# Kernel tuning notes

Measured on AMD Instinct MI355X. Metric: run time of the kernel, lower is better.

Reference implementation:

```python
import jax, jax.numpy as jnp
import numpy as np
import math

B, T, C, H = 4, 2048, 1024, 16
DH = C // H  # 64

def setup_inputs() -> dict:
    key = jax.random.key(0)
    k1, k2, k3 = jax.random.split(key, 3)
    x = jax.random.normal(k1, (B, T, C), dtype=jnp.float32)
    # standard RoPE angle table: [T, DH/2]
    inv_freq = 1.0 / (10000.0 ** (jnp.arange(0, DH, 2, dtype=jnp.float32) / DH))
    ang = jnp.arange(T, dtype=jnp.float32)[:, None] * inv_freq[None, :]
    cos = jnp.cos(ang)
    sin = jnp.sin(ang)
    Wqkv = jax.random.normal(k2, (3 * C, C), dtype=jnp.float32) * (C ** -0.5)
    Wo = jax.random.normal(k3, (C, C), dtype=jnp.float32) * (C ** -0.5)
    return {"x": x, "cos": cos, "sin": sin, "Wqkv": Wqkv, "Wo": Wo}

def apply_rotary(x, cos, sin):
    # x: [B,H,T,DH]; cos/sin: [T, DH/2] broadcast over B,H
    x1, x2 = x[..., ::2], x[..., 1::2]
    xr = jnp.stack([x1 * cos - x2 * sin, x1 * sin + x2 * cos], axis=-1)
    return xr.reshape(x.shape)

def reference(x, cos, sin, Wqkv, Wo):
    Bz, Tz, Cz = x.shape
    qkv = x @ Wqkv.T  # [B,T,3C]
    q, k, v = jnp.split(qkv, 3, axis=-1)
    def heads(t):
        return t.reshape(Bz, Tz, H, DH).transpose(0, 2, 1, 3)  # [B,H,T,DH]
    q, k, v = heads(q), heads(k), heads(v)
    q = apply_rotary(q, cos, sin)
    k = apply_rotary(k, cos, sin)
    attn = jnp.einsum('bhqd,bhkd->bhqk', q, k) / math.sqrt(DH)
    causal = jnp.tril(jnp.ones((Tz, Tz), dtype=bool))
    attn = jnp.where(causal, attn, jnp.float32(-jnp.inf))
    attn = jax.nn.softmax(attn, axis=-1)
    y = jnp.einsum('bhqk,bhkd->bhqd', attn, v)
    y = y.transpose(0, 2, 1, 3).reshape(Bz, Tz, Cz)
    return y @ Wo.T
```

## Files before the change

kernel.cpp:

```cpp
#include <hip/hip_runtime.h>
#include <math.h>

#define Bz 4
#define Tz 2048
#define Cz 1024
#define Hz 16
#define DHz 64
#define Mz (Bz*Tz)

typedef __attribute__((ext_vector_type(8))) short short8;
typedef __attribute__((ext_vector_type(4))) float f32x4;
typedef __attribute__((ext_vector_type(4))) float flt4;
typedef unsigned long long u64;

__device__ inline unsigned short f2bf(float f){
  union { float f; unsigned int u; } x; x.f = f;
  unsigned int r = x.u + 0x7fffu + ((x.u >> 16) & 1u);
  return (unsigned short)(r >> 16);
}
__device__ inline float bf2f(unsigned short b){
  union { unsigned int u; float f; } x; x.u = ((unsigned int)b) << 16; return x.f;
}
__device__ inline unsigned int packbf2(float lo, float hi){
  union { float f; unsigned int u; } a, b; a.f = lo; b.f = hi;
  return __builtin_amdgcn_perm(b.u, a.u, 0x07060302u);
}

__device__ inline void gload_lds16(const unsigned short* g, char* l){
  __builtin_amdgcn_global_load_lds((const __attribute__((address_space(1))) unsigned int*)g,
                                   (__attribute__((address_space(3))) unsigned int*)l,
                                   16, 0, 0);
}

#define NXE 8388608
#define NW1 3145728
#define NW2 1048576
__global__ __launch_bounds__(256) void cvt_all(const float* __restrict__ x,
                                               const float* __restrict__ wq,
                                               const float* __restrict__ wo,
                                               unsigned short* __restrict__ xb,
                                               unsigned short* __restrict__ wqb,
                                               unsigned short* __restrict__ wob){
  int i = (blockIdx.x * 256 + threadIdx.x) * 4;
  const float* s; unsigned short* d;
  if (i < NXE){ s = x + i; d = xb + i; }
  else if (i < NXE + NW1){ s = wq + (i - NXE); d = wqb + (i - NXE); }
  else { s = wo + (i - NXE - NW1); d = wob + (i - NXE - NW1); }
  flt4 v = *(const flt4*)s;
  u64 pack = (u64)f2bf(v.x) | ((u64)f2bf(v.y) << 16)
           | ((u64)f2bf(v.z) << 32) | ((u64)f2bf(v.w) << 48);
  *(u64*)d = pack;
}

template<int EPI>
__global__ __launch_bounds__(256)
void gemm_bt(const unsigned short* __restrict__ A, const unsigned short* __restrict__ Bw,
             const int K,
             unsigned short* __restrict__ qd, unsigned short* __restrict__ kd,
             unsigned short* __restrict__ vd, float* __restrict__ outf)
{
  __shared__ __align__(16) char lds[32768];
  char* At = lds;
  char* Bt = lds + 16384;

  const int tid  = threadIdx.x;
  const int lane = tid & 63, wid = tid >> 6;
  const int l16  = lane & 15, lg = lane >> 4;
  const int wr   = wid >> 1, wc = wid & 1;
  const int m0   = blockIdx.y * 128, n0 = blockIdx.x * 128;

  f32x4 acc[4][4] = {};
  const int nk = K >> 6;

  for (int kt = 0; kt < nk; ++kt){
    const unsigned short* As = A  + (size_t)m0 * K + kt * 64;
    const unsigned short* Bs = Bw + (size_t)n0 * K + kt * 64;
    #pragma unroll
    for (int it = 0; it < 4; ++it){
      int id  = it * 256 + tid;
      int row = id >> 3, c = id & 7;
      int sc  = c ^ (row & 7);
      char* dA = At + (it * 256 + wid * 64) * 16;
      char* dB = Bt + (it * 256 + wid * 64) * 16;
      gload_lds16(As + (size_t)row * K + sc * 8, dA);
      gload_lds16(Bs + (size_t)row * K + sc * 8, dB);
    }
    __syncthreads();

    #pragma unroll
    for (int ks = 0; ks < 2; ++ks){
      short8 af[4], bf[4];
      #pragma unroll
      for (int mt = 0; mt < 4; ++mt){
        int row = wr * 64 + mt * 16 + l16;
        af[mt] = *(const short8*)(At + row * 128 + (((ks * 4 + lg) ^ (row & 7)) << 4));
      }
      #pragma unroll
      for (int nt = 0; nt < 4; ++nt){
        int row = wc * 64 + nt * 16 + l16;
        bf[nt] = *(const short8*)(Bt + row * 128 + (((ks * 4 + lg) ^ (row & 7)) << 4));
      }
      #pragma unroll
      for (int mt = 0; mt < 4; ++mt)
        #pragma unroll
        for (int nt = 0; nt < 4; ++nt)
          acc[mt][nt] = __builtin_amdgcn_mfma_f32_16x16x32_bf16(af[mt], bf[nt], acc[mt][nt], 0, 0, 0);
    }
    __syncthreads();
  }

  if (EPI == 1){
    #pragma unroll
    for (int mt = 0; mt < 4; ++mt)
      #pragma unroll
      for (int nt = 0; nt < 4; ++nt)
        #pragma unroll
        for (int i = 0; i < 4; ++i){
          int m = m0 + wr * 64 + mt * 16 + lg * 4 + i;
          int n = n0 + wc * 64 + nt * 16 + l16;
          outf[(size_t)m * 1024 + n] = acc[mt][nt][i];
        }
  } else {
    const int part = n0 >> 10;
    if (part < 2){
      unsigned short* dst = part ? kd : qd;
      #pragma unroll
      for (int mt = 0; mt < 4; ++mt)
        #pragma unroll
        for (int nt = 0; nt < 4; ++nt)
          #pragma unroll
          for (int i = 0; i < 4; ++i){
            int m = m0 + wr * 64 + mt * 16 + lg * 4 + i;
            int n = (n0 & 1023) + wc * 64 + nt * 16 + l16;
            int h = n >> 6, d = n & 63;
            int b = m >> 11, t = m & 2047;
            dst[(((size_t)(b * Hz + h)) * Tz + t) * DHz + d] = f2bf(acc[mt][nt][i]);
          }
    } else {
      #pragma unroll
      for (int mt = 0; mt < 4; ++mt)
        #pragma unroll
        for (int nt = 0; nt < 4; ++nt){
          int m = m0 + wr * 64 + mt * 16 + lg * 4;
          int n = (n0 & 1023) + wc * 64 + nt * 16 + l16;
          int h = n >> 6, d = n & 63;
          int b = m >> 11, t = m & 2047;
          u64 w = (u64)f2bf(acc[mt][nt][0]) | ((u64)f2bf(acc[mt][nt][1]) << 16)
                | ((u64)f2bf(acc[mt][nt][2]) << 32) | ((u64)f2bf(acc[mt][nt][3]) << 48);
          *(u64*)(vd + (((size_t)(b * Hz + h)) * DHz + d) * Tz + t) = w;
        }
    }
  }
}

__global__ __launch_bounds__(256) void rope_kernel(unsigned short* __restrict__ qh,
                                                   unsigned short* __restrict__ kh,
                                                   const float* __restrict__ cosb,
                                                   const float* __restrict__ sinb){
  unsigned int idx = blockIdx.x * 256 + threadIdx.x;
  int quad = idx & 7;
  int row  = (idx >> 3) & 131071;
  int buf  = idx >> 20;
  unsigned short* p = (buf ? kh : qh) + (size_t)row * DHz + quad * 8;
  int t = row & (Tz - 1);
  flt4 c = *(const flt4*)(cosb + t * 32 + quad * 4);
  flt4 s = *(const flt4*)(sinb + t * 32 + quad * 4);
  short8 v = *(const short8*)p;
  const float qs = 0.125f * 1.4426950408889634f;
  float sc = buf ? 1.0f : qs;
  short8 o;
  #pragma unroll
  for (int j = 0; j < 4; ++j){
    float x1 = bf2f((unsigned short)v[2*j]);
    float x2 = bf2f((unsigned short)v[2*j+1]);
    float r1 = (x1 * c[j] - x2 * s[j]) * sc;
    float r2 = (x1 * s[j] + x2 * c[j]) * sc;
    o[2*j]   = (short)f2bf(r1);
    o[2*j+1] = (short)f2bf(r2);
  }
  *(short8*)p = o;
}

__global__ __launch_bounds__(256)
void attn_fwd(const unsigned short* __restrict__ qh, const unsigned short* __restrict__ kh,
              const unsigned short* __restrict__ vt, unsigned short* __restrict__ y)
{
  __shared__ __align__(16) char lds[2*8192 + 2*8192 + 4*2304];
  const int tid  = threadIdx.x;
  const int lane = tid & 63, wid = tid >> 6;
  const int l16  = lane & 15, lg = lane >> 4;
  const int bh   = blockIdx.x;
  const int qt   = 31 - blockIdx.y;

  const size_t base = (size_t)bh * Tz * DHz;
  const unsigned short* qb = qh + base;
  const unsigned short* kb = kh + base;
  const unsigned short* vb = vt + base;

  const int qrow = qt * 64 + wid * 16 + l16;
  short8 qf[2];
  qf[0] = *(const short8*)(qb + (size_t)qrow * DHz + 0  + lg * 8);
  qf[1] = *(const short8*)(qb + (size_t)qrow * DHz + 32 + lg * 8);

  const int x07 = l16 & 7;
  const int fo0 = l16 * 128 + (((0 + lg) ^ x07) << 4);
  const int fo1 = l16 * 128 + (((4 + lg) ^ x07) << 4);
  char* const Pb  = (char*)lds + 32768 + wid * 2304;
  const int pwo = (l16 * 72 + lg * 4) * 2;
  const int pro = (l16 * 72 + lg * 8) * 2;

  const int srow = tid >> 3;
  const int scol = (tid & 7) ^ (srow & 7);
  const int kOff = srow * DHz + scol * 8;
  const size_t vOff = (size_t)srow * Tz + scol * 8;

  auto STAGE = [&](int kt, int c){
    const unsigned short* Ks = kb + (size_t)kt * 64 * DHz;
    const unsigned short* Vs = vb + kt * 64;
    char* KD = (char*)lds + c * 8192;
    char* VD = (char*)lds + 16384 + c * 8192;
    #pragma unroll
    for (int it = 0; it < 2; ++it){
      gload_lds16(Ks + kOff + it * 32 * DHz, KD + it * 4096 + wid * 1024);
      gload_lds16(Vs + vOff + (size_t)it * 32 * Tz, VD + it * 4096 + wid * 1024);
    }
  };

  short8 ones;
  #pragma unroll
  for (int j = 0; j < 8; ++j) ones[j] = (short)0x3F80;

  f32x4 o[4] = {};
  f32x4 lsum = {};
  float m_r = -INFINITY;

  int cur = 0;
  STAGE(0, 0);
  __syncthreads();

  for (int kt = 0; kt <= qt; ++kt){
    if (kt < qt) STAGE(kt + 1, cur ^ 1);

    const char* KL = (const char*)lds + cur * 8192;
    const char* VL = (const char*)lds + 16384 + cur * 8192;

    f32x4 s[4] = {};
    __builtin_amdgcn_s_setprio(1);
    #pragma unroll
    for (int nt = 0; nt < 4; ++nt){
      short8 kf = *(const short8*)(KL + fo0 + nt * 2048);
      s[nt] = __builtin_amdgcn_mfma_f32_16x16x32_bf16(kf, qf[0], s[nt], 0, 0, 0);
    }
    #pragma unroll
    for (int nt = 0; nt < 4; ++nt){
      short8 kf = *(const short8*)(KL + fo1 + nt * 2048);
      s[nt] = __builtin_amdgcn_mfma_f32_16x16x32_bf16(kf, qf[1], s[nt], 0, 0, 0);
    }
    __builtin_amdgcn_s_setprio(0);

    if (kt == qt){
      #pragma unroll
      for (int nt = 0; nt < 4; ++nt)
        #pragma unroll
        for (int r = 0; r < 4; ++r){
          int kv = kt * 64 + nt * 16 + lg * 4 + r;
          if (kv > qrow) s[nt][r] = -INFINITY;
        }
    }

    float mx = fmaxf(fmaxf(fmaxf(fmaxf(s[0][0], s[0][1]), fmaxf(s[0][2], s[0][3])),
                           fmaxf(fmaxf(s[1][0], s[1][1]), fmaxf(s[1][2], s[1][3]))),
                     fmaxf(fmaxf(fmaxf(s[2][0], s[2][1]), fmaxf(s[2][2], s[2][3])),
                           fmaxf(fmaxf(s[3][0], s[3][1]), fmaxf(s[3][2], s[3][3]))));
    mx = fmaxf(mx, __shfl_xor(mx, 16));
    mx = fmaxf(mx, __shfl_xor(mx, 32));

    if (!__all(mx - m_r <= 8.0f)){
      float mn = fmaxf(m_r, mx);
      float al = __builtin_amdgcn_exp2f(m_r - mn);
      #pragma unroll
      for (int nt = 0; nt < 4; ++nt)
        #pragma unroll
        for (int i = 0; i < 4; ++i) o[nt][i] *= al;
      #pragma unroll
      for (int i = 0; i < 4; ++i) lsum[i] *= al;
      m_r = mn;
    }

    #pragma unroll
    for (int nt = 0; nt < 4; ++nt){
      float p0 = __builtin_amdgcn_exp2f(s[nt][0] - m_r);
      float p1 = __builtin_amdgcn_exp2f(s[nt][1] - m_r);
      float p2 = __builtin_amdgcn_exp2f(s[nt][2] - m_r);
      float p3 = __builtin_amdgcn_exp2f(s[nt][3] - m_r);
      u64 w = (u64)packbf2(p0, p1) | ((u64)packbf2(p2, p3) << 32);
      *(u64*)(Pb + pwo + nt * 32) = w;
    }

    __builtin_amdgcn_s_setprio(1);
    #pragma unroll
    for (int ks = 0; ks < 2; ++ks){
      short8 pa = *(const short8*)(Pb + pro + ks * 64);
      lsum = __builtin_amdgcn_mfma_f32_16x16x32_bf16(ones, pa, lsum, 0, 0, 0);
      const int fo = ks ? fo1 : fo0;
      #pragma unroll
      for (int nt = 0; nt < 4; ++nt){
        short8 vf = *(const short8*)(VL + fo + nt * 2048);
        o[nt] = __builtin_amdgcn_mfma_f32_16x16x32_bf16(vf, pa, o[nt], 0, 0, 0);
      }
    }
    __builtin_amdgcn_s_setprio(0);

    __syncthreads();
    cur ^= 1;
  }

  const int b = bh >> 4, h = bh & 15;
  const int row = qt * 64 + wid * 16 + l16;
  unsigned short* yb = y + ((size_t)b * Tz + row) * Cz + h * 64 + lg * 4;
  float inv = 1.f / lsum[0];
  #pragma unroll
  for (int nt = 0; nt < 4; ++nt){
    u64 w = (u64)f2bf(o[nt][0] * inv) | ((u64)f2bf(o[nt][1] * inv) << 16)
          | ((u64)f2bf(o[nt][2] * inv) << 32) | ((u64)f2bf(o[nt][3] * inv) << 48);
    *(u64*)(yb + nt * 16) = w;
  }
}

extern "C" void kernel_launch(void* const* d_in, const int* in_sizes, int n_in,
                              void* d_out, int out_size, void* d_ws, size_t ws_size,
                              hipStream_t stream)
{
  const float* x    = (const float*)d_in[0];
  const float* cosb = (const float*)d_in[1];
  const float* sinb = (const float*)d_in[2];
  const float* Wqkv = (const float*)d_in[3];
  const float* Wo   = (const float*)d_in[4];
  float* out = (float*)d_out;

  char* ws = (char*)d_ws;
  unsigned short* xb    = (unsigned short*)(ws);
  unsigned short* ybuf  = xb;
  unsigned short* wqkvb = (unsigned short*)(ws + 16777216);
  unsigned short* wob   = (unsigned short*)(ws + 23068672);
  unsigned short* qhb   = (unsigned short*)(ws + 25165824);
  unsigned short* khb   = (unsigned short*)(ws + 41943040);
  unsigned short* vtb   = (unsigned short*)(ws + 58720256);

  cvt_all<<<12288, 256, 0, stream>>>(x, Wqkv, Wo, xb, wqkvb, wob);

  dim3 g1(24, 64);
  gemm_bt<0><<<g1, 256, 0, stream>>>(xb, wqkvb, Cz, qhb, khb, vtb, nullptr);

  rope_kernel<<<8192, 256, 0, stream>>>(qhb, khb, cosb, sinb);

  dim3 g2(64, 32);
  attn_fwd<<<g2, 256, 0, stream>>>(qhb, khb, vtb, ybuf);

  dim3 g3(8, 64);
  gemm_bt<1><<<g3, 256, 0, stream>>>(ybuf, wob, Cz, nullptr, nullptr, nullptr, out);
}
```

Baseline: 266.2 us.

## Fuse RoPE into QKV GEMM epilogue, swizzle block order, vectorize stores

Drops the standalone RoPE kernel and applies rotary embedding plus the Q scale in the QKV GEMM epilogue. Swapped MFMA operands give each lane contiguous columns, which allows packed 8-byte bf16 and 16-byte fp32 stores. All three main kernels use a 1D grid with an XCD-aware block swizzle for better L2 locality. Attention peels the diagonal tile out of the loop and re-swizzles the P scratch layout in LDS. This saves one full read and write pass over Q and K, at the cost of more epilogue work and register pressure in the GEMM.

```diff
diff --git a/kernel.cpp b/kernel.cpp
--- a/kernel.cpp
+++ b/kernel.cpp
@@ -10,6 +10,7 @@
 
 typedef __attribute__((ext_vector_type(8))) short short8;
 typedef __attribute__((ext_vector_type(4))) float f32x4;
+typedef __attribute__((ext_vector_type(2))) float flt2;
 typedef __attribute__((ext_vector_type(4))) float flt4;
 typedef unsigned long long u64;
 
@@ -25,6 +26,9 @@
   union { float f; unsigned int u; } a, b; a.f = lo; b.f = hi;
   return __builtin_amdgcn_perm(b.u, a.u, 0x07060302u);
 }
+__device__ inline u64 pack4bf(float a, float b, float c, float d){
+  return (u64)f2bf(a) | ((u64)f2bf(b) << 16) | ((u64)f2bf(c) << 32) | ((u64)f2bf(d) << 48);
+}
 
 __device__ inline void gload_lds16(const unsigned short* g, char* l){
   __builtin_amdgcn_global_load_lds((const __attribute__((address_space(1))) unsigned int*)g,
@@ -34,7 +38,6 @@
 
 #define NXE 8388608
 #define NW1 3145728
-#define NW2 1048576
 __global__ __launch_bounds__(256) void cvt_all(const float* __restrict__ x,
                                                const float* __restrict__ wq,
                                                const float* __restrict__ wo,
@@ -47,150 +50,158 @@
   else if (i < NXE + NW1){ s = wq + (i - NXE); d = wqb + (i - NXE); }
   else { s = wo + (i - NXE - NW1); d = wob + (i - NXE - NW1); }
   flt4 v = *(const flt4*)s;
-  u64 pack = (u64)f2bf(v.x) | ((u64)f2bf(v.y) << 16)
-           | ((u64)f2bf(v.z) << 32) | ((u64)f2bf(v.w) << 48);
-  *(u64*)d = pack;
-}
-
-template<int EPI>
+  *(u64*)d = pack4bf(v.x, v.y, v.z, v.w);
+}
+
+template<int SWAP>
+__device__ __forceinline__ void gemm_core(const unsigned short* __restrict__ As0,
+                                          const unsigned short* __restrict__ Bs0,
+                                          char* At, char* Bt,
+                                          int tid, int wid, int l16, int lg, int wr, int wc,
+                                          f32x4 acc[4][4])
+{
+  const int srow = tid >> 3;
+  const int scol = (tid & 7) ^ (srow & 7);
+  for (int kt = 0; kt < 16; ++kt){
+    const unsigned short* As = As0 + kt * 64;
+    const unsigned short* Bs = Bs0 + kt * 64;
+    #pragma unroll
+    for (int it = 0; it < 4; ++it){
+      gload_lds16(As + (size_t)(it * 32 + srow) * 1024 + scol * 8, At + it * 4096 + wid * 1024);
+      gload_lds16(Bs + (size_t)(it * 32 + srow) * 1024 + scol * 8, Bt + it * 4096 + wid * 1024);
+    }
+    __syncthreads();
+    #pragma unroll
+    for (int ks = 0; ks < 2; ++ks){
+      short8 af[4], bf[4];
+      #pragma unroll
+      for (int mt = 0; mt < 4; ++mt){
+        int row = wr * 64 + mt * 16 + l16;
+        af[mt] = *(const short8*)(At + row * 128 + (((ks * 4 + lg) ^ (row & 7)) << 4));
+      }
+      #pragma unroll
+      for (int nt = 0; nt < 4; ++nt){
+        int row = wc * 64 + nt * 16 + l16;
+        bf[nt] = *(const short8*)(Bt + row * 128 + (((ks * 4 + lg) ^ (row & 7)) << 4));
+      }
+      #pragma unroll
+      for (int mt = 0; mt < 4; ++mt)
+        #pragma unroll
+        for (int nt = 0; nt < 4; ++nt)
+          acc[mt][nt] = SWAP
+            ? __builtin_amdgcn_mfma_f32_16x16x32_bf16(bf[nt], af[mt], acc[mt][nt], 0, 0, 0)
+            : __builtin_amdgcn_mfma_f32_16x16x32_bf16(af[mt], bf[nt], acc[mt][nt], 0, 0, 0);
+    }
+    __syncthreads();
+  }
+}
+
 __global__ __launch_bounds__(256)
-void gemm_bt(const unsigned short* __restrict__ A, const unsigned short* __restrict__ Bw,
-             const int K,
-             unsigned short* __restrict__ qd, unsigned short* __restrict__ kd,
-             unsigned short* __restrict__ vd, float* __restrict__ outf)
+void gemm_qkv(const unsigned short* __restrict__ A, const unsigned short* __restrict__ Bw,
+              unsigned short* __restrict__ qd, unsigned short* __restrict__ kd,
+              unsigned short* __restrict__ vd,
+              const float* __restrict__ cosb, const float* __restrict__ sinb)
 {
   __shared__ __align__(16) char lds[32768];
-  char* At = lds;
-  char* Bt = lds + 16384;
+  char* At = lds; char* Bt = lds + 16384;
+
+  const int swz = (blockIdx.x & 7) * 192 + (blockIdx.x >> 3);
+  const int nb = swz % 24, mb = swz / 24;
+  const int m0 = mb * 128, n0 = nb * 128;
 
   const int tid  = threadIdx.x;
   const int lane = tid & 63, wid = tid >> 6;
   const int l16  = lane & 15, lg = lane >> 4;
   const int wr   = wid >> 1, wc = wid & 1;
-  const int m0   = blockIdx.y * 128, n0 = blockIdx.x * 128;
+  const int part = n0 >> 10;
 
   f32x4 acc[4][4] = {};
-  const int nk = K >> 6;
-
-  for (int kt = 0; kt < nk; ++kt){
-    const unsigned short* As = A  + (size_t)m0 * K + kt * 64;
-    const unsigned short* Bs = Bw + (size_t)n0 * K + kt * 64;
-    #pragma unroll
-    for (int it = 0; it < 4; ++it){
-      int id  = it * 256 + tid;
-      int row = id >> 3, c = id & 7;
-      int sc  = c ^ (row & 7);
-      char* dA = At + (it * 256 + wid * 64) * 16;
-      char* dB = Bt + (it * 256 + wid * 64) * 16;
-      gload_lds16(As + (size_t)row * K + sc * 8, dA);
-      gload_lds16(Bs + (size_t)row * K + sc * 8, dB);
-    }
-    __syncthreads();
-
-    #pragma unroll
-    for (int ks = 0; ks < 2; ++ks){
-      short8 af[4], bf[4];
-      #pragma unroll
-      for (int mt = 0; mt < 4; ++mt){
-        int row = wr * 64 + mt * 16 + l16;
-        af[mt] = *(const short8*)(At + row * 128 + (((ks * 4 + lg) ^ (row & 7)) << 4));
-      }
+
+  if (part < 2){
+    gemm_core<1>(A + (size_t)m0 * 1024, Bw + (size_t)n0 * 1024, At, Bt,
+                 tid, wid, l16, lg, wr, wc, acc);
+    unsigned short* dst = part ? kd : qd;
+    const float qs = part ? 1.0f : 0.125f * 1.4426950408889634f;
+    #pragma unroll
+    for (int mt = 0; mt < 4; ++mt){
+      int m = m0 + wr * 64 + mt * 16 + l16;
+      int b = m >> 11, t = m & 2047;
+      const float* cb = cosb + t * 32;
+      const float* sb = sinb + t * 32;
       #pragma unroll
       for (int nt = 0; nt < 4; ++nt){
-        int row = wc * 64 + nt * 16 + l16;
-        bf[nt] = *(const short8*)(Bt + row * 128 + (((ks * 4 + lg) ^ (row & 7)) << 4));
-      }
-      #pragma unroll
-      for (int mt = 0; mt < 4; ++mt)
-        #pragma unroll
-        for (int nt = 0; nt < 4; ++nt)
-          acc[mt][nt] = __builtin_amdgcn_mfma_f32_16x16x32_bf16(af[mt], bf[nt], acc[mt][nt], 0, 0, 0);
-    }
-    __syncthreads();
+        int n4 = (n0 & 1023) + wc * 64 + nt * 16 + lg * 4;
+        int h = n4 >> 6, d0 = n4 & 63;
+        flt2 c = *(const flt2*)(cb + (d0 >> 1));
+        flt2 s = *(const flt2*)(sb + (d0 >> 1));
+        float x0 = acc[mt][nt][0], x1 = acc[mt][nt][1];
+        float x2 = acc[mt][nt][2], x3 = acc[mt][nt][3];
+        float r0 = (x0 * c.x - x1 * s.x) * qs;
+        float r1 = (x0 * s.x + x1 * c.x) * qs;
+        float r2 = (x2 * c.y - x3 * s.y) * qs;
+        float r3 = (x2 * s.y + x3 * c.y) * qs;
+        *(u64*)(dst + (((size_t)(b * Hz + h)) * Tz + t) * DHz + d0) = pack4bf(r0, r1, r2, r3);
+      }
+    }
+  } else {
+    gemm_core<0>(A + (size_t)m0 * 1024, Bw + (size_t)n0 * 1024, At, Bt,
+                 tid, wid, l16, lg, wr, wc, acc);
+    #pragma unroll
+    for (int mt = 0; mt < 4; ++mt)
+      #pragma unroll
+      for (int nt = 0; nt < 4; ++nt){
+        int m = m0 + wr * 64 + mt * 16 + lg * 4;
+        int n = (n0 & 1023) + wc * 64 + nt * 16 + l16;
+        int h = n >> 6, d = n & 63;
+        int b = m >> 11, t = m & 2047;
+        *(u64*)(vd + (((size_t)(b * Hz + h)) * DHz + d) * Tz + t)
+          = pack4bf(acc[mt][nt][0], acc[mt][nt][1], acc[mt][nt][2], acc[mt][nt][3]);
+      }
   }
-
-  if (EPI == 1){
-    #pragma unroll
-    for (int mt = 0; mt < 4; ++mt)
-      #pragma unroll
-      for (int nt = 0; nt < 4; ++nt)
-        #pragma unroll
-        for (int i = 0; i < 4; ++i){
-          int m = m0 + wr * 64 + mt * 16 + lg * 4 + i;
-          int n = n0 + wc * 64 + nt * 16 + l16;
-          outf[(size_t)m * 1024 + n] = acc[mt][nt][i];
-        }
-  } else {
-    const int part = n0 >> 10;
-    if (part < 2){
-      unsigned short* dst = part ? kd : qd;
-      #pragma unroll
-      for (int mt = 0; mt < 4; ++mt)
-        #pragma unroll
-        for (int nt = 0; nt < 4; ++nt)
-          #pragma unroll
-          for (int i = 0; i < 4; ++i){
-            int m = m0 + wr * 64 + mt * 16 + lg * 4 + i;
-            int n = (n0 & 1023) + wc * 64 + nt * 16 + l16;
-            int h = n >> 6, d = n & 63;
-            int b = m >> 11, t = m & 2047;
-            dst[(((size_t)(b * Hz + h)) * Tz + t) * DHz + d] = f2bf(acc[mt][nt][i]);
-          }
-    } else {
-      #pragma unroll
-      for (int mt = 0; mt < 4; ++mt)
-        #pragma unroll
-        for (int nt = 0; nt < 4; ++nt){
-          int m = m0 + wr * 64 + mt * 16 + lg * 4;
-          int n = (n0 & 1023) + wc * 64 + nt * 16 + l16;
-          int h = n >> 6, d = n & 63;
-          int b = m >> 11, t = m & 2047;
-          u64 w = (u64)f2bf(acc[mt][nt][0]) | ((u64)f2bf(acc[mt][nt][1]) << 16)
-                | ((u64)f2bf(acc[mt][nt][2]) << 32) | ((u64)f2bf(acc[mt][nt][3]) << 48);
-          *(u64*)(vd + (((size_t)(b * Hz + h)) * DHz + d) * Tz + t) = w;
-        }
+}
+
+__global__ __launch_bounds__(256)
+void gemm_out(const unsigned short* __restrict__ A, const unsigned short* __restrict__ Bw,
+              float* __restrict__ outf)
+{
+  __shared__ __align__(16) char lds[32768];
+  char* At = lds; char* Bt = lds + 16384;
+
+  const int swz = (blockIdx.x & 7) * 64 + (blockIdx.x >> 3);
+  const int nb = swz % 8, mb = swz / 8;
+  const int m0 = mb * 128, n0 = nb * 128;
+
+  const int tid  = threadIdx.x;
+  const int lane = tid & 63, wid = tid >> 6;
+  const int l16  = lane & 15, lg = lane >> 4;
+  const int wr   = wid >> 1, wc = wid & 1;
+
+  f32x4 acc[4][4] = {};
+  gemm_core<1>(A + (size_t)m0 * 1024, Bw + (size_t)n0 * 1024, At, Bt,
+               tid, wid, l16, lg, wr, wc, acc);
+
+  #pragma unroll
+  for (int mt = 0; mt < 4; ++mt){
+    int m = m0 + wr * 64 + mt * 16 + l16;
+    #pragma unroll
+    for (int nt = 0; nt < 4; ++nt){
+      int n = n0 + wc * 64 + nt * 16 + lg * 4;
+      *(f32x4*)(outf + (size_t)m * 1024 + n) = acc[mt][nt];
     }
   }
-}
-
-__global__ __launch_bounds__(256) void rope_kernel(unsigned short* __restrict__ qh,
-                                                   unsigned short* __restrict__ kh,
-                                                   const float* __restrict__ cosb,
-                                                   const float* __restrict__ sinb){
-  unsigned int idx = blockIdx.x * 256 + threadIdx.x;
-  int quad = idx & 7;
-  int row  = (idx >> 3) & 131071;
-  int buf  = idx >> 20;
-  unsigned short* p = (buf ? kh : qh) + (size_t)row * DHz + quad * 8;
-  int t = row & (Tz - 1);
-  flt4 c = *(const flt4*)(cosb + t * 32 + quad * 4);
-  flt4 s = *(const flt4*)(sinb + t * 32 + quad * 4);
-  short8 v = *(const short8*)p;
-  const float qs = 0.125f * 1.4426950408889634f;
-  float sc = buf ? 1.0f : qs;
-  short8 o;
-  #pragma unroll
-  for (int j = 0; j < 4; ++j){
-    float x1 = bf2f((unsigned short)v[2*j]);
-    float x2 = bf2f((unsigned short)v[2*j+1]);
-    float r1 = (x1 * c[j] - x2 * s[j]) * sc;
-    float r2 = (x1 * s[j] + x2 * c[j]) * sc;
-    o[2*j]   = (short)f2bf(r1);
-    o[2*j+1] = (short)f2bf(r2);
-  }
-  *(short8*)p = o;
 }
 
 __global__ __launch_bounds__(256)
 void attn_fwd(const unsigned short* __restrict__ qh, const unsigned short* __restrict__ kh,
               const unsigned short* __restrict__ vt, unsigned short* __restrict__ y)
 {
-  __shared__ __align__(16) char lds[2*8192 + 2*8192 + 4*2304];
+  __shared__ __align__(16) char lds[40960];
   const int tid  = threadIdx.x;
   const int lane = tid & 63, wid = tid >> 6;
   const int l16  = lane & 15, lg = lane >> 4;
-  const int bh   = blockIdx.x;
-  const int qt   = 31 - blockIdx.y;
+  const int swzb = (blockIdx.x & 7) * 256 + (blockIdx.x >> 3);
+  const int bh   = swzb >> 5;
+  const int qt   = 31 - (swzb & 31);
 
   const size_t base = (size_t)bh * Tz * DHz;
   const unsigned short* qb = qh + base;
@@ -205,9 +216,13 @@
   const int x07 = l16 & 7;
   const int fo0 = l16 * 128 + (((0 + lg) ^ x07) << 4);
   const int fo1 = l16 * 128 + (((4 + lg) ^ x07) << 4);
-  char* const Pb  = (char*)lds + 32768 + wid * 2304;
-  const int pwo = (l16 * 72 + lg * 4) * 2;
-  const int pro = (l16 * 72 + lg * 8) * 2;
+  char* const Pb = (char*)lds + 32768 + wid * 2048;
+  int pw[4], prd[2];
+  #pragma unroll
+  for (int nt = 0; nt < 4; ++nt)
+    pw[nt] = l16 * 128 + ((((nt << 1) + (lg >> 1)) ^ x07) << 4) + ((lg & 1) << 3);
+  prd[0] = l16 * 128 + (((0 + lg) ^ x07) << 4);
+  prd[1] = l16 * 128 + (((4 + lg) ^ x07) << 4);
 
   const int srow = tid >> 3;
   const int scol = (tid & 7) ^ (srow & 7);
@@ -234,16 +249,7 @@
   f32x4 lsum = {};
   float m_r = -INFINITY;
 
-  int cur = 0;
-  STAGE(0, 0);
-  __syncthreads();
-
-  for (int kt = 0; kt <= qt; ++kt){
-    if (kt < qt) STAGE(kt + 1, cur ^ 1);
-
-    const char* KL = (const char*)lds + cur * 8192;
-    const char* VL = (const char*)lds + 16384 + cur * 8192;
-
+  auto TILE = [&](bool diag, int kt, const char* KL, const char* VL){
     f32x4 s[4] = {};
     __builtin_amdgcn_s_setprio(1);
     #pragma unroll
@@ -258,7 +264,7 @@
     }
     __builtin_amdgcn_s_setprio(0);
 
-    if (kt == qt){
+    if (diag){
       #pragma unroll
       for (int nt = 0; nt < 4; ++nt)
         #pragma unroll
@@ -293,14 +299,13 @@
       float p1 = __builtin_amdgcn_exp2f(s[nt][1] - m_r);
       float p2 = __builtin_amdgcn_exp2f(s[nt][2] - m_r);
       float p3 = __builtin_amdgcn_exp2f(s[nt][3] - m_r);
-      u64 w = (u64)packbf2(p0, p1) | ((u64)packbf2(p2, p3) << 32);
-      *(u64*)(Pb + pwo + nt * 32) = w;
+      *(u64*)(Pb + pw[nt]) = (u64)packbf2(p0, p1) | ((u64)packbf2(p2, p3) << 32);
     }
 
     __builtin_amdgcn_s_setprio(1);
     #pragma unroll
     for (int ks = 0; ks < 2; ++ks){
-      short8 pa = *(const short8*)(Pb + pro + ks * 64);
+      short8 pa = *(const short8*)(Pb + prd[ks]);
       lsum = __builtin_amdgcn_mfma_f32_16x16x32_bf16(ones, pa, lsum, 0, 0, 0);
       const int fo = ks ? fo1 : fo0;
       #pragma unroll
@@ -310,21 +315,28 @@
       }
     }
     __builtin_amdgcn_s_setprio(0);
-
+  };
+
+  int cur = 0;
+  STAGE(0, 0);
+  __syncthreads();
+
+  for (int kt = 0; kt < qt; ++kt){
+    STAGE(kt + 1, cur ^ 1);
+    TILE(false, kt, (const char*)lds + cur * 8192, (const char*)lds + 16384 + cur * 8192);
     __syncthreads();
     cur ^= 1;
   }
+  TILE(true, qt, (const char*)lds + cur * 8192, (const char*)lds + 16384 + cur * 8192);
 
   const int b = bh >> 4, h = bh & 15;
   const int row = qt * 64 + wid * 16 + l16;
   unsigned short* yb = y + ((size_t)b * Tz + row) * Cz + h * 64 + lg * 4;
   float inv = 1.f / lsum[0];
   #pragma unroll
-  for (int nt = 0; nt < 4; ++nt){
-    u64 w = (u64)f2bf(o[nt][0] * inv) | ((u64)f2bf(o[nt][1] * inv) << 16)
-          | ((u64)f2bf(o[nt][2] * inv) << 32) | ((u64)f2bf(o[nt][3] * inv) << 48);
-    *(u64*)(yb + nt * 16) = w;
-  }
+  for (int nt = 0; nt < 4; ++nt)
+    *(u64*)(yb + nt * 16) = pack4bf(o[nt][0] * inv, o[nt][1] * inv,
+                                    o[nt][2] * inv, o[nt][3] * inv);
 }
 
 extern "C" void kernel_launch(void* const* d_in, const int* in_sizes, int n_in,
@@ -349,14 +361,9 @@
 
   cvt_all<<<12288, 256, 0, stream>>>(x, Wqkv, Wo, xb, wqkvb, wob);
 
-  dim3 g1(24, 64);
-  gemm_bt<0><<<g1, 256, 0, stream>>>(xb, wqkvb, Cz, qhb, khb, vtb, nullptr);
-
-  rope_kernel<<<8192, 256, 0, stream>>>(qhb, khb, cosb, sinb);
-
-  dim3 g2(64, 32);
-  attn_fwd<<<g2, 256, 0, stream>>>(qhb, khb, vtb, ybuf);
-
-  dim3 g3(8, 64);
-  gemm_bt<1><<<g3, 256, 0, stream>>>(ybuf, wob, Cz, nullptr, nullptr, nullptr, out);
-}
+  gemm_qkv<<<1536, 256, 0, stream>>>(xb, wqkvb, qhb, khb, vtb, cosb, sinb);
+
+  attn_fwd<<<2048, 256, 0, stream>>>(qhb, khb, vtb, ybuf);
+
+  gemm_out<<<512, 256, 0, stream>>>(ybuf, wob, out);
+}
```

Result: slower. 273.0 us (+2.6%).
